# Performance work log

Hardware: AMD Instinct MI355X
Metric: run time of the kernel (lower is better)

The kernel has to match this reference:

```python
import jax, jax.numpy as jnp
import numpy as np

N_NODES = 100000
N_EDGES = 1600000
N_FEAT = 128
HIDDEN = 64
N_CLASSES = 16


def setup_inputs() -> dict:
    key = jax.random.key(0)
    ks = jax.random.split(key, 8)
    x = jax.random.normal(ks[0], (N_NODES, N_FEAT), dtype=jnp.float32)
    edge_index = jax.random.randint(ks[1], (2, N_EDGES), 0, N_NODES, dtype=jnp.int64)
    def glorot(k, shape):
        lim = float(np.sqrt(6.0 / (shape[0] + shape[1])))
        return jax.random.uniform(k, shape, jnp.float32, -lim, lim)
    return {
        "x": x,
        "edge_index": edge_index,
        "W0": glorot(ks[2], (N_FEAT, HIDDEN)), "b0": jnp.zeros((HIDDEN,), jnp.float32),
        "W1": glorot(ks[3], (HIDDEN, HIDDEN)), "b1": jnp.zeros((HIDDEN,), jnp.float32),
        "W2": glorot(ks[4], (HIDDEN, 2)),      "b2": jnp.zeros((2,), jnp.float32),
        "Wc": glorot(ks[5], (2, N_CLASSES)),   "bc": jnp.zeros((N_CLASSES,), jnp.float32),
    }


def _gcn_conv(x, W, b, src, dst, norm, n_nodes):
    # GCNConv: D^{-1/2} (A + I) D^{-1/2} X W + b, edges already include self-loops
    h = x @ W                                  # transform first (small dim)
    msg = h[src] * norm[:, None]               # gather + per-edge scale
    agg = jax.ops.segment_sum(msg, dst, num_segments=n_nodes)  # scatter-add
    return agg + b


def reference(x, edge_index, W0, b0, W1, b1, W2, b2, Wc, bc):
    n = x.shape[0]
    loops = jnp.arange(n, dtype=edge_index.dtype)
    src = jnp.concatenate([edge_index[0], loops])
    dst = jnp.concatenate([edge_index[1], loops])
    # degree on destination (col), including self-loops
    deg = jax.ops.segment_sum(jnp.ones_like(dst, dtype=x.dtype), dst, num_segments=n)
    dis = jnp.where(deg > 0, jax.lax.rsqrt(deg), 0.0)
    norm = dis[src] * dis[dst]

    h = _gcn_conv(x, W0, b0, src, dst, norm, n)              # layer 0, no activation
    h = jnp.tanh(_gcn_conv(h, W1, b1, src, dst, norm, n))    # layer 1
    h = jnp.tanh(_gcn_conv(h, W2, b2, src, dst, norm, n))    # layer 2 -> [N, 2]
    embeddings = h
    out = embeddings @ Wc + bc                               # [N, num_classes]
    return (out, embeddings)
```

## Files before the change

kernel.cpp:

```cpp
#include <hip/hip_runtime.h>


#define NF 128
#define NH 64
#define NPB 256
#define MAXNB 512
#define CAP 6144
#define A1G 1024

__global__ void k_init0(const int* __restrict__ ei, int* __restrict__ fmt,
                        int* __restrict__ ccnt, int nb16) {
    int i = blockIdx.x * 256 + threadIdx.x;
    if (i < nb16) ccnt[i] = 0;
    if (i == 0) {
        int f = 1;
        #pragma unroll
        for (int k = 1; k < 32; k += 2) if (ei[k] != 0) f = 0;
        *fmt = f;
    }
}

__global__ void __launch_bounds__(256) k_coarse(
        const int* __restrict__ ei, const int* __restrict__ fmt,
        int* __restrict__ ccnt, int* __restrict__ blockbase, int E, int NB) {
    __shared__ int h[MAXNB];
    int sh = *fmt;
    for (int i = threadIdx.x; i < NB; i += 256) h[i] = 0;
    __syncthreads();
    for (long long e = (long long)blockIdx.x * 256 + threadIdx.x; e < E;
         e += (long long)A1G * 256) {
        int d = ei[(long long)(E + e) << sh];
        atomicAdd(&h[d >> 8], 1);
    }
    __syncthreads();
    for (int b = threadIdx.x; b < NB; b += 256) {
        int c = h[b];
        int base = (c > 0) ? atomicAdd(&ccnt[b * 16], c) : 0;
        blockbase[(long long)blockIdx.x * NB + b] = base;
    }
}

__global__ void __launch_bounds__(512) k_cscan(
        const int* __restrict__ ccnt, int* __restrict__ cstart, int NB) {
    __shared__ int s[512];
    int t = threadIdx.x;
    int c = (t < NB) ? ccnt[t * 16] : 0;
    s[t] = c;
    __syncthreads();
    for (int off = 1; off < 512; off <<= 1) {
        int v = s[t];
        int u = (t >= off) ? s[t - off] : 0;
        __syncthreads();
        s[t] = v + u;
        __syncthreads();
    }
    if (t < NB) cstart[t] = s[t] - c;
}

__global__ void __launch_bounds__(256) k_cscatter(
        const int* __restrict__ ei, const int* __restrict__ fmt,
        const int* __restrict__ cstart, const int* __restrict__ blockbase,
        int* __restrict__ pairs, int E, int NB) {
    __shared__ int h[MAXNB];
    __shared__ int bb[MAXNB];
    int sh = *fmt;
    for (int i = threadIdx.x; i < NB; i += 256) {
        h[i] = 0;
        bb[i] = cstart[i] + blockbase[(long long)blockIdx.x * NB + i];
    }
    __syncthreads();
    for (long long e = (long long)blockIdx.x * 256 + threadIdx.x; e < E;
         e += (long long)A1G * 256) {
        int s = ei[(long long)e << sh];
        int d = ei[(long long)(E + e) << sh];
        int b = d >> 8;
        int r = atomicAdd(&h[b], 1);
        pairs[bb[b] + r] = s | ((d & 255) << 17);
    }
}

__global__ void __launch_bounds__(256) k_bucket(
        const int* __restrict__ pairs, const int* __restrict__ ccnt,
        const int* __restrict__ cstart, int* __restrict__ esrc,
        int* __restrict__ cnt, int* __restrict__ start, float* __restrict__ dis,
        int N) {
    __shared__ int words[CAP];
    __shared__ unsigned char rk[CAP];
    __shared__ int h[NPB];
    __shared__ int hs[NPB];
    int b = blockIdx.x;
    int cs = cstart[b];
    int ec = ccnt[b * 16];
    if (ec > CAP) ec = CAP;
    int t = threadIdx.x;
    for (int i = t; i < ec; i += 256) words[i] = pairs[cs + i];
    h[t] = 0;
    __syncthreads();
    for (int i = t; i < ec; i += 256) {
        int ld = words[i] >> 17;
        rk[i] = (unsigned char)atomicAdd(&h[ld], 1);
    }
    __syncthreads();
    int c = h[t];
    hs[t] = c;
    __syncthreads();
    for (int off = 1; off < 256; off <<= 1) {
        int v = hs[t];
        int u = (t >= off) ? hs[t - off] : 0;
        __syncthreads();
        hs[t] = v + u;
        __syncthreads();
    }
    int node = b * NPB + t;
    if (node < N) {
        cnt[node] = c;
        start[node] = cs + hs[t] - c;
        dis[node] = rsqrtf(1.0f + (float)c);
    }
    for (int i = t; i < ec; i += 256) {
        int w = words[i];
        int ld = w >> 17;
        esrc[cs + (hs[ld] - h[ld]) + rk[i]] = w & 0x1FFFF;
    }
}

#define KP3 68
__global__ void __launch_bounds__(256) k_gemm128(
        const float* __restrict__ X, const float* __restrict__ W,
        const float* __restrict__ dis, short* __restrict__ T16,
        float* __restrict__ rs, int n) {
    __shared__ float xs[64 * KP3];
    __shared__ float Ws[64 * NH];
    __shared__ int rmax[64];
    if (threadIdx.x < 64) rmax[threadIdx.x] = 0;
    long long rowbase = (long long)blockIdx.x * 64;
    int c0 = (threadIdx.x & 15) * 4;
    int r0 = (threadIdx.x >> 4) * 4;
    float4 a0{0,0,0,0}, a1{0,0,0,0}, a2{0,0,0,0}, a3{0,0,0,0};
    #pragma unroll
    for (int ph = 0; ph < 2; ++ph) {
        if (ph) __syncthreads();
        const float4* Wp4 = (const float4*)(W + (long long)ph * 64 * NH);
        for (int i = threadIdx.x; i < 64 * NH / 4; i += 256)
            ((float4*)Ws)[i] = Wp4[i];
        const float* Xp = X + rowbase * NF + ph * 64;
        for (int i = threadIdx.x; i < 1024; i += 256) {
            int r = i >> 4, kk = (i & 15) << 2;
            float4 v = (rowbase + r < n)
                           ? *(const float4*)(Xp + r * NF + kk)
                           : make_float4(0.f, 0.f, 0.f, 0.f);
            *(float4*)&xs[r * KP3 + kk] = v;
        }
        __syncthreads();
        const float* x0 = &xs[(r0 + 0) * KP3];
        const float* x1 = &xs[(r0 + 1) * KP3];
        const float* x2 = &xs[(r0 + 2) * KP3];
        const float* x3 = &xs[(r0 + 3) * KP3];
        const float* Wp0 = &Ws[c0];
        #pragma unroll 4
        for (int k4 = 0; k4 < 16; ++k4) {
            float4 xv0 = *(const float4*)(x0 + k4 * 4);
            float4 xv1 = *(const float4*)(x1 + k4 * 4);
            float4 xv2 = *(const float4*)(x2 + k4 * 4);
            float4 xv3 = *(const float4*)(x3 + k4 * 4);
            float4 wa = *(const float4*)(Wp0 + (k4 * 4 + 0) * NH);
            float4 wb = *(const float4*)(Wp0 + (k4 * 4 + 1) * NH);
            float4 wc = *(const float4*)(Wp0 + (k4 * 4 + 2) * NH);
            float4 wd = *(const float4*)(Wp0 + (k4 * 4 + 3) * NH);
            a0.x += xv0.x * wa.x; a0.y += xv0.x * wa.y; a0.z += xv0.x * wa.z; a0.w += xv0.x * wa.w;
            a1.x += xv1.x * wa.x; a1.y += xv1.x * wa.y; a1.z += xv1.x * wa.z; a1.w += xv1.x * wa.w;
            a2.x += xv2.x * wa.x; a2.y += xv2.x * wa.y; a2.z += xv2.x * wa.z; a2.w += xv2.x * wa.w;
            a3.x += xv3.x * wa.x; a3.y += xv3.x * wa.y; a3.z += xv3.x * wa.z; a3.w += xv3.x * wa.w;
            a0.x += xv0.y * wb.x; a0.y += xv0.y * wb.y; a0.z += xv0.y * wb.z; a0.w += xv0.y * wb.w;
            a1.x += xv1.y * wb.x; a1.y += xv1.y * wb.y; a1.z += xv1.y * wb.z; a1.w += xv1.y * wb.w;
            a2.x += xv2.y * wb.x; a2.y += xv2.y * wb.y; a2.z += xv2.y * wb.z; a2.w += xv2.y * wb.w;
            a3.x += xv3.y * wb.x; a3.y += xv3.y * wb.y; a3.z += xv3.y * wb.z; a3.w += xv3.y * wb.w;
            a0.x += xv0.z * wc.x; a0.y += xv0.z * wc.y; a0.z += xv0.z * wc.z; a0.w += xv0.z * wc.w;
            a1.x += xv1.z * wc.x; a1.y += xv1.z * wc.y; a1.z += xv1.z * wc.z; a1.w += xv1.z * wc.w;
            a2.x += xv2.z * wc.x; a2.y += xv2.z * wc.y; a2.z += xv2.z * wc.z; a2.w += xv2.z * wc.w;
            a3.x += xv3.z * wc.x; a3.y += xv3.z * wc.y; a3.z += xv3.z * wc.z; a3.w += xv3.z * wc.w;
            a0.x += xv0.w * wd.x; a0.y += xv0.w * wd.y; a0.z += xv0.w * wd.z; a0.w += xv0.w * wd.w;
            a1.x += xv1.w * wd.x; a1.y += xv1.w * wd.y; a1.z += xv1.w * wd.z; a1.w += xv1.w * wd.w;
            a2.x += xv2.w * wd.x; a2.y += xv2.w * wd.y; a2.z += xv2.w * wd.z; a2.w += xv2.w * wd.w;
            a3.x += xv3.w * wd.x; a3.y += xv3.w * wd.y; a3.z += xv3.w * wd.z; a3.w += xv3.w * wd.w;
        }
    }
    int row = (int)rowbase + r0;
    float d0 = (row + 0 < n) ? dis[row + 0] : 0.0f;
    float d1 = (row + 1 < n) ? dis[row + 1] : 0.0f;
    float d2 = (row + 2 < n) ? dis[row + 2] : 0.0f;
    float d3 = (row + 3 < n) ? dis[row + 3] : 0.0f;
    a0.x *= d0; a0.y *= d0; a0.z *= d0; a0.w *= d0;
    a1.x *= d1; a1.y *= d1; a1.z *= d1; a1.w *= d1;
    a2.x *= d2; a2.y *= d2; a2.z *= d2; a2.w *= d2;
    a3.x *= d3; a3.y *= d3; a3.z *= d3; a3.w *= d3;
    float m0 = fmaxf(fmaxf(fabsf(a0.x), fabsf(a0.y)), fmaxf(fabsf(a0.z), fabsf(a0.w)));
    float m1 = fmaxf(fmaxf(fabsf(a1.x), fabsf(a1.y)), fmaxf(fabsf(a1.z), fabsf(a1.w)));
    float m2 = fmaxf(fmaxf(fabsf(a2.x), fabsf(a2.y)), fmaxf(fabsf(a2.z), fabsf(a2.w)));
    float m3 = fmaxf(fmaxf(fabsf(a3.x), fabsf(a3.y)), fmaxf(fabsf(a3.z), fabsf(a3.w)));
    atomicMax(&rmax[r0 + 0], __float_as_int(m0));
    atomicMax(&rmax[r0 + 1], __float_as_int(m1));
    atomicMax(&rmax[r0 + 2], __float_as_int(m2));
    atomicMax(&rmax[r0 + 3], __float_as_int(m3));
    __syncthreads();
    float M0 = __int_as_float(rmax[r0 + 0]);
    float M1 = __int_as_float(rmax[r0 + 1]);
    float M2 = __int_as_float(rmax[r0 + 2]);
    float M3 = __int_as_float(rmax[r0 + 3]);
    float i0 = 32767.0f / fmaxf(M0, 1e-20f);
    float i1 = 32767.0f / fmaxf(M1, 1e-20f);
    float i2 = 32767.0f / fmaxf(M2, 1e-20f);
    float i3 = 32767.0f / fmaxf(M3, 1e-20f);
    const float ks = 1.0f / 32767.0f;
    if (row + 0 < n) {
        short4 q = { (short)__float2int_rn(a0.x * i0), (short)__float2int_rn(a0.y * i0),
                     (short)__float2int_rn(a0.z * i0), (short)__float2int_rn(a0.w * i0) };
        *(short4*)&T16[(long long)(row + 0) * NH + c0] = q;
        if (c0 == 0) rs[row + 0] = M0 * ks;
    }
    if (row + 1 < n) {
        short4 q = { (short)__float2int_rn(a1.x * i1), (short)__float2int_rn(a1.y * i1),
                     (short)__float2int_rn(a1.z * i1), (short)__float2int_rn(a1.w * i1) };
        *(short4*)&T16[(long long)(row + 1) * NH + c0] = q;
        if (c0 == 0) rs[row + 1] = M1 * ks;
    }
    if (row + 2 < n) {
        short4 q = { (short)__float2int_rn(a2.x * i2), (short)__float2int_rn(a2.y * i2),
                     (short)__float2int_rn(a2.z * i2), (short)__float2int_rn(a2.w * i2) };
        *(short4*)&T16[(long long)(row + 2) * NH + c0] = q;
        if (c0 == 0) rs[row + 2] = M2 * ks;
    }
    if (row + 3 < n) {
        short4 q = { (short)__float2int_rn(a3.x * i3), (short)__float2int_rn(a3.y * i3),
                     (short)__float2int_rn(a3.z * i3), (short)__float2int_rn(a3.w * i3) };
        *(short4*)&T16[(long long)(row + 3) * NH + c0] = q;
        if (c0 == 0) rs[row + 3] = M3 * ks;
    }
}

#define EDGE_A(J) {                                                           \
    int s_ = __builtin_amdgcn_readlane(sA, (J));                              \
    float f_ = __int_as_float(__builtin_amdgcn_readlane(fAb, (J)));           \
    accA = fmaf(f_, (float)(T + s_ * NH)[lane], accA); }
#define EDGE_B(J) {                                                           \
    int s_ = __builtin_amdgcn_readlane(sB, (J));                              \
    float f_ = __int_as_float(__builtin_amdgcn_readlane(fBb, (J)));           \
    accB = fmaf(f_, (float)(T + s_ * NH)[lane], accB); }

#define SEG_GATHER2                                                           \
    int lane = threadIdx.x & 63;                                              \
    int na = blockIdx.x * 8 + (threadIdx.x >> 6) * 2;                         \
    int nb_ = na + 1;                                                         \
    if (na >= n) return;                                                      \
    bool hasB = (nb_ < n);                                                    \
    float dia = dis[na];                                                      \
    float dib = hasB ? dis[nb_] : 0.0f;                                       \
    int ga = cnt[na], sta = start[na];                                        \
    int gb = hasB ? cnt[nb_] : 0;                                             \
    int stb = hasB ? start[nb_] : 0;                                          \
    float accA = rs[na] * (float)T[na * NH + lane];                           \
    float accB = hasB ? rs[nb_] * (float)T[nb_ * NH + lane] : 0.0f;           \
    int gmax = ga > gb ? ga : gb;                                             \
    for (int base = 0; base < gmax; base += 64) {                             \
        int ma = ga - base; ma = ma < 0 ? 0 : (ma > 64 ? 64 : ma);            \
        int mb = gb - base; mb = mb < 0 ? 0 : (mb > 64 ? 64 : mb);            \
        int sA = 0, sB = 0; float fA = 0.0f, fB = 0.0f;                       \
        if (lane < ma) { sA = esrc[sta + base + lane]; fA = rs[sA]; }         \
        if (lane < mb) { sB = esrc[stb + base + lane]; fB = rs[sB]; }         \
        int fAb = __float_as_int(fA), fBb = __float_as_int(fB);               \
        int mmin = ma < mb ? ma : mb;                                         \
        int j = 0;                                                            \
        for (; j + 3 < mmin; j += 4) {                                        \
            EDGE_A(j + 0) EDGE_B(j + 0)                                       \
            EDGE_A(j + 1) EDGE_B(j + 1)                                       \
            EDGE_A(j + 2) EDGE_B(j + 2)                                       \
            EDGE_A(j + 3) EDGE_B(j + 3)                                       \
        }                                                                     \
        int jA = j, jB = j;                                                   \
        for (; jA + 3 < ma; jA += 4) {                                        \
            EDGE_A(jA + 0) EDGE_A(jA + 1) EDGE_A(jA + 2) EDGE_A(jA + 3)       \
        }                                                                     \
        for (; jA < ma; ++jA) EDGE_A(jA)                                      \
        for (; jB + 3 < mb; jB += 4) {                                        \
            EDGE_B(jB + 0) EDGE_B(jB + 1) EDGE_B(jB + 2) EDGE_B(jB + 3)       \
        }                                                                     \
        for (; jB < mb; ++jB) EDGE_B(jB)                                      \
    }

__global__ void __launch_bounds__(256) k_seg0t(
        const short* __restrict__ T, const float* __restrict__ rs,
        const int* __restrict__ esrc, const int* __restrict__ start,
        const int* __restrict__ cnt, const float* __restrict__ dis,
        const float* __restrict__ b0, const float* __restrict__ W1,
        short* __restrict__ To, float* __restrict__ rso, int n) {
    __shared__ float W1s[NH * NH];
    for (int i = threadIdx.x; i < NH * NH / 4; i += 256)
        ((float4*)W1s)[i] = ((const float4*)W1)[i];
    __syncthreads();
    SEG_GATHER2
    float bv = b0[lane];
    float hA = dia * accA + bv;
    float hB = dib * accB + bv;
    float oA = 0.0f, oB = 0.0f;
    #pragma unroll
    for (int c = 0; c < 64; ++c) {
        float wv = W1s[c * NH + lane];
        float ha = __int_as_float(__builtin_amdgcn_readlane(__float_as_int(hA), c));
        float hb = __int_as_float(__builtin_amdgcn_readlane(__float_as_int(hB), c));
        oA = fmaf(ha, wv, oA);
        oB = fmaf(hb, wv, oB);
    }
    oA *= dia;
    oB *= dib;
    float mA = fabsf(oA), mB = fabsf(oB);
    #pragma unroll
    for (int msk = 32; msk; msk >>= 1) {
        mA = fmaxf(mA, __shfl_xor(mA, msk, 64));
        mB = fmaxf(mB, __shfl_xor(mB, msk, 64));
    }
    float iA = 32767.0f / fmaxf(mA, 1e-20f);
    float iB = 32767.0f / fmaxf(mB, 1e-20f);
    const float ks = 1.0f / 32767.0f;
    To[(long long)na * NH + lane] = (short)__float2int_rn(oA * iA);
    if (lane == 0) rso[na] = mA * ks;
    if (hasB) {
        To[(long long)nb_ * NH + lane] = (short)__float2int_rn(oB * iB);
        if (lane == 0) rso[nb_] = mB * ks;
    }
}

__global__ void __launch_bounds__(256) k_seg1f(
        const short* __restrict__ T, const float* __restrict__ rs,
        const int* __restrict__ esrc, const int* __restrict__ start,
        const int* __restrict__ cnt, const float* __restrict__ dis,
        const float* __restrict__ b1, const float* __restrict__ W2,
        float2* __restrict__ t2, int n) {
    SEG_GATHER2
    float bv = b1[lane];
    float2 w = ((const float2*)W2)[lane];
    float tA = tanhf(dia * accA + bv);
    float p0 = tA * w.x, p1 = tA * w.y;
    float tB = hasB ? tanhf(dib * accB + bv) : 0.0f;
    float q0 = tB * w.x, q1 = tB * w.y;
    #pragma unroll
    for (int msk = 32; msk; msk >>= 1) {
        p0 += __shfl_xor(p0, msk, 64);
        p1 += __shfl_xor(p1, msk, 64);
        q0 += __shfl_xor(q0, msk, 64);
        q1 += __shfl_xor(q1, msk, 64);
    }
    if (lane == 0) {
        t2[na] = make_float2(dia * p0, dia * p1);
        if (hasB) t2[nb_] = make_float2(dib * q0, dib * q1);
    }
}

__global__ void __launch_bounds__(256) k_seg2f(
        const float2* __restrict__ T2, const int* __restrict__ esrc,
        const int* __restrict__ start, const int* __restrict__ cnt,
        const float* __restrict__ dis, const float* __restrict__ b2,
        const float* __restrict__ Wc, const float* __restrict__ bc,
        float* __restrict__ out, float* __restrict__ emb, int n) {
    __shared__ float Wcs[32];
    __shared__ float bcs[16];
    if (threadIdx.x < 32) Wcs[threadIdx.x] = Wc[threadIdx.x];
    if (threadIdx.x < 16) bcs[threadIdx.x] = bc[threadIdx.x];
    __syncthreads();
    int i = blockIdx.x * 256 + threadIdx.x;
    if (i >= n) return;
    float di = dis[i];
    int g = cnt[i], st = start[i];
    float2 self = T2[i];
    float a0 = self.x, a1 = self.y;
    int j = 0;
    for (; j + 7 < g; j += 8) {
        int e0 = esrc[st+j],   e1 = esrc[st+j+1], e2 = esrc[st+j+2], e3 = esrc[st+j+3];
        int e4 = esrc[st+j+4], e5 = esrc[st+j+5], e6 = esrc[st+j+6], e7 = esrc[st+j+7];
        float2 v0 = T2[e0], v1 = T2[e1], v2 = T2[e2], v3 = T2[e3];
        float2 v4 = T2[e4], v5 = T2[e5], v6 = T2[e6], v7 = T2[e7];
        a0 += v0.x + v1.x + v2.x + v3.x + v4.x + v5.x + v6.x + v7.x;
        a1 += v0.y + v1.y + v2.y + v3.y + v4.y + v5.y + v6.y + v7.y;
    }
    for (; j < g; ++j) {
        float2 v = T2[esrc[st + j]];
        a0 += v.x; a1 += v.y;
    }
    float e0 = tanhf(a0 * di + b2[0]);
    float e1 = tanhf(a1 * di + b2[1]);
    *(float2*)&emb[(long long)i * 2] = make_float2(e0, e1);
    float* op = &out[(long long)i * 16];
    #pragma unroll
    for (int c4 = 0; c4 < 4; ++c4) {
        float4 o;
        o.x = e0 * Wcs[c4*4+0] + e1 * Wcs[16 + c4*4+0] + bcs[c4*4+0];
        o.y = e0 * Wcs[c4*4+1] + e1 * Wcs[16 + c4*4+1] + bcs[c4*4+1];
        o.z = e0 * Wcs[c4*4+2] + e1 * Wcs[16 + c4*4+2] + bcs[c4*4+2];
        o.w = e0 * Wcs[c4*4+3] + e1 * Wcs[16 + c4*4+3] + bcs[c4*4+3];
        *(float4*)&op[c4 * 4] = o;
    }
}

extern "C" void kernel_launch(void* const* d_in, const int* in_sizes, int n_in,
                              void* d_out, int out_size, void* d_ws, size_t ws_size,
                              hipStream_t stream) {
    const float* x  = (const float*)d_in[0];
    const int*   ei = (const int*)  d_in[1];
    const float* W0 = (const float*)d_in[2];
    const float* b0 = (const float*)d_in[3];
    const float* W1 = (const float*)d_in[4];
    const float* b1 = (const float*)d_in[5];
    const float* W2 = (const float*)d_in[6];
    const float* b2 = (const float*)d_in[7];
    const float* Wc = (const float*)d_in[8];
    const float* bc = (const float*)d_in[9];

    int N = in_sizes[0] / NF;
    int E = in_sizes[1] / 2;
    int NB = (N + NPB - 1) / NPB;

    float* out = (float*)d_out;
    float* emb = out + (long long)N * 16;

    short*  T16a = (short*)d_ws;
    char*   r2   = (char*)d_ws + (long long)N * NH * 2;
    short*  T16b = (short*)r2;
    float2* t2   = (float2*)(r2 + (long long)N * NH * 2);
    float*  rs_b = (float*)(r2 + (long long)N * NH * 2 + (long long)N * 8);
    float*  dis  = (float*)((char*)d_ws + (long long)N * NH * 2 + (long long)N * NH * 4);
    float*  rs_a = dis + N;
    int*    cnt   = (int*)(rs_a + N);
    int*    start = cnt + N;
    int*    esrc  = start + N;
    int*    fmt   = esrc + E;

    int* pairs     = (int*)d_ws;
    int* blockbase = pairs + E;
    int* ccnt      = blockbase + (long long)A1G * NB;
    int* cstart    = ccnt + NB * 16;

    int nb_n  = (N + 255) / 256;
    int nb_g  = (N + 63) / 64;
    int nb_s2 = (N + 7) / 8;
    int nb_i0 = (NB * 16 + 255) / 256;

    k_init0   <<<nb_i0, 256, 0, stream>>>(ei, fmt, ccnt, NB * 16);
    k_coarse  <<<A1G, 256, 0, stream>>>(ei, fmt, ccnt, blockbase, E, NB);
    k_cscan   <<<1, 512, 0, stream>>>(ccnt, cstart, NB);
    k_cscatter<<<A1G, 256, 0, stream>>>(ei, fmt, cstart, blockbase, pairs, E, NB);
    k_bucket  <<<NB, 256, 0, stream>>>(pairs, ccnt, cstart, esrc, cnt, start, dis, N);

    k_gemm128 <<<nb_g, 256, 0, stream>>>(x, W0, dis, T16a, rs_a, N);

    k_seg0t   <<<nb_s2, 256, 0, stream>>>(T16a, rs_a, esrc, start, cnt, dis, b0,
                                          W1, T16b, rs_b, N);

    k_seg1f   <<<nb_s2, 256, 0, stream>>>(T16b, rs_b, esrc, start, cnt, dis, b1,
                                          W2, t2, N);

    k_seg2f   <<<nb_n, 256, 0, stream>>>(t2, esrc, start, cnt, dis, b2, Wc, bc,
                                         out, emb, N);
}
```

Before: 333.3 us.

## Prefetch second GEMM phase, persistent seg0 grid, 16-lane parallel seg2 gather

The first GEMM now issues global loads for both K-halves up front, holding the second half in registers while the first is computed, and sets a 4-blocks-per-CU launch bound. The layer-1 aggregation kernel becomes grid-stride over a capped grid of 2048 blocks so the shared W1 load is amortised across many nodes. The final 2-wide aggregation spreads each node's edges across 16 lanes and combines them with shuffles, replacing one serial thread per node. These target memory-latency exposure and per-block setup, at the cost of more registers in the GEMM and less parallel slack in seg0.

```diff
diff --git a/kernel.cpp b/kernel.cpp
--- a/kernel.cpp
+++ b/kernel.cpp
@@ -124,8 +124,47 @@
     }
 }
 
+#define GEMM_K4_BODY                                                          \
+            float4 xv0 = *(const float4*)(x0 + k4 * 4);                       \
+            float4 xv1 = *(const float4*)(x1 + k4 * 4);                       \
+            float4 xv2 = *(const float4*)(x2 + k4 * 4);                       \
+            float4 xv3 = *(const float4*)(x3 + k4 * 4);                       \
+            float4 wa = *(const float4*)(Wp0 + (k4 * 4 + 0) * NH);            \
+            float4 wb = *(const float4*)(Wp0 + (k4 * 4 + 1) * NH);            \
+            float4 wc = *(const float4*)(Wp0 + (k4 * 4 + 2) * NH);            \
+            float4 wd = *(const float4*)(Wp0 + (k4 * 4 + 3) * NH);            \
+            a0.x += xv0.x * wa.x; a0.y += xv0.x * wa.y; a0.z += xv0.x * wa.z; a0.w += xv0.x * wa.w; \
+            a1.x += xv1.x * wa.x; a1.y += xv1.x * wa.y; a1.z += xv1.x * wa.z; a1.w += xv1.x * wa.w; \
+            a2.x += xv2.x * wa.x; a2.y += xv2.x * wa.y; a2.z += xv2.x * wa.z; a2.w += xv2.x * wa.w; \
+            a3.x += xv3.x * wa.x; a3.y += xv3.x * wa.y; a3.z += xv3.x * wa.z; a3.w += xv3.x * wa.w; \
+            a0.x += xv0.y * wb.x; a0.y += xv0.y * wb.y; a0.z += xv0.y * wb.z; a0.w += xv0.y * wb.w; \
+            a1.x += xv1.y * wb.x; a1.y += xv1.y * wb.y; a1.z += xv1.y * wb.z; a1.w += xv1.y * wb.w; \
+            a2.x += xv2.y * wb.x; a2.y += xv2.y * wb.y; a2.z += xv2.y * wb.z; a2.w += xv2.y * wb.w; \
+            a3.x += xv3.y * wb.x; a3.y += xv3.y * wb.y; a3.z += xv3.y * wb.z; a3.w += xv3.y * wb.w; \
+            a0.x += xv0.z * wc.x; a0.y += xv0.z * wc.y; a0.z += xv0.z * wc.z; a0.w += xv0.z * wc.w; \
+            a1.x += xv1.z * wc.x; a1.y += xv1.z * wc.y; a1.z += xv1.z * wc.z; a1.w += xv1.z * wc.w; \
+            a2.x += xv2.z * wc.x; a2.y += xv2.z * wc.y; a2.z += xv2.z * wc.z; a2.w += xv2.z * wc.w; \
+            a3.x += xv3.z * wc.x; a3.y += xv3.z * wc.y; a3.z += xv3.z * wc.z; a3.w += xv3.z * wc.w; \
+            a0.x += xv0.w * wd.x; a0.y += xv0.w * wd.y; a0.z += xv0.w * wd.z; a0.w += xv0.w * wd.w; \
+            a1.x += xv1.w * wd.x; a1.y += xv1.w * wd.y; a1.z += xv1.w * wd.z; a1.w += xv1.w * wd.w; \
+            a2.x += xv2.w * wd.x; a2.y += xv2.w * wd.y; a2.z += xv2.w * wd.z; a2.w += xv2.w * wd.w; \
+            a3.x += xv3.w * wd.x; a3.y += xv3.w * wd.y; a3.z += xv3.w * wd.z; a3.w += xv3.w * wd.w;
+
+#define GEMM_PHASE_COMPUTE                                                    \
+    {                                                                         \
+        const float* x0 = &xs[(r0 + 0) * KP3];                                \
+        const float* x1 = &xs[(r0 + 1) * KP3];                                \
+        const float* x2 = &xs[(r0 + 2) * KP3];                                \
+        const float* x3 = &xs[(r0 + 3) * KP3];                                \
+        const float* Wp0 = &Ws[c0];                                           \
+        _Pragma("unroll 4")                                                   \
+        for (int k4 = 0; k4 < 16; ++k4) {                                     \
+            GEMM_K4_BODY                                                      \
+        }                                                                     \
+    }
+
 #define KP3 68
-__global__ void __launch_bounds__(256) k_gemm128(
+__global__ void __launch_bounds__(256, 4) k_gemm128(
         const float* __restrict__ X, const float* __restrict__ W,
         const float* __restrict__ dis, short* __restrict__ T16,
         float* __restrict__ rs, int n) {
@@ -134,57 +173,43 @@
     __shared__ int rmax[64];
     if (threadIdx.x < 64) rmax[threadIdx.x] = 0;
     long long rowbase = (long long)blockIdx.x * 64;
-    int c0 = (threadIdx.x & 15) * 4;
-    int r0 = (threadIdx.x >> 4) * 4;
+    int tid = threadIdx.x;
+    int c0 = (tid & 15) * 4;
+    int r0 = (tid >> 4) * 4;
+    const float4* W4 = (const float4*)W;
+    #pragma unroll
+    for (int u = 0; u < 4; ++u) {
+        int i = tid + u * 256;
+        int r = i >> 4, kk = (i & 15) << 2;
+        float4 xv = (rowbase + r < n)
+                        ? *(const float4*)(X + (rowbase + r) * NF + kk)
+                        : make_float4(0.f, 0.f, 0.f, 0.f);
+        *(float4*)&xs[r * KP3 + kk] = xv;
+        ((float4*)Ws)[i] = W4[i];
+    }
+    float4 x1r[4], w1r[4];
+    #pragma unroll
+    for (int u = 0; u < 4; ++u) {
+        int i = tid + u * 256;
+        int r = i >> 4, kk = (i & 15) << 2;
+        x1r[u] = (rowbase + r < n)
+                     ? *(const float4*)(X + (rowbase + r) * NF + 64 + kk)
+                     : make_float4(0.f, 0.f, 0.f, 0.f);
+        w1r[u] = W4[1024 + i];
+    }
     float4 a0{0,0,0,0}, a1{0,0,0,0}, a2{0,0,0,0}, a3{0,0,0,0};
+    __syncthreads();
+    GEMM_PHASE_COMPUTE
+    __syncthreads();
     #pragma unroll
-    for (int ph = 0; ph < 2; ++ph) {
-        if (ph) __syncthreads();
-        const float4* Wp4 = (const float4*)(W + (long long)ph * 64 * NH);
-        for (int i = threadIdx.x; i < 64 * NH / 4; i += 256)
-            ((float4*)Ws)[i] = Wp4[i];
-        const float* Xp = X + rowbase * NF + ph * 64;
-        for (int i = threadIdx.x; i < 1024; i += 256) {
-            int r = i >> 4, kk = (i & 15) << 2;
-            float4 v = (rowbase + r < n)
-                           ? *(const float4*)(Xp + r * NF + kk)
-                           : make_float4(0.f, 0.f, 0.f, 0.f);
-            *(float4*)&xs[r * KP3 + kk] = v;
-        }
-        __syncthreads();
-        const float* x0 = &xs[(r0 + 0) * KP3];
-        const float* x1 = &xs[(r0 + 1) * KP3];
-        const float* x2 = &xs[(r0 + 2) * KP3];
-        const float* x3 = &xs[(r0 + 3) * KP3];
-        const float* Wp0 = &Ws[c0];
-        #pragma unroll 4
-        for (int k4 = 0; k4 < 16; ++k4) {
-            float4 xv0 = *(const float4*)(x0 + k4 * 4);
-            float4 xv1 = *(const float4*)(x1 + k4 * 4);
-            float4 xv2 = *(const float4*)(x2 + k4 * 4);
-            float4 xv3 = *(const float4*)(x3 + k4 * 4);
-            float4 wa = *(const float4*)(Wp0 + (k4 * 4 + 0) * NH);
-            float4 wb = *(const float4*)(Wp0 + (k4 * 4 + 1) * NH);
-            float4 wc = *(const float4*)(Wp0 + (k4 * 4 + 2) * NH);
-            float4 wd = *(const float4*)(Wp0 + (k4 * 4 + 3) * NH);
-            a0.x += xv0.x * wa.x; a0.y += xv0.x * wa.y; a0.z += xv0.x * wa.z; a0.w += xv0.x * wa.w;
-            a1.x += xv1.x * wa.x; a1.y += xv1.x * wa.y; a1.z += xv1.x * wa.z; a1.w += xv1.x * wa.w;
-            a2.x += xv2.x * wa.x; a2.y += xv2.x * wa.y; a2.z += xv2.x * wa.z; a2.w += xv2.x * wa.w;
-            a3.x += xv3.x * wa.x; a3.y += xv3.x * wa.y; a3.z += xv3.x * wa.z; a3.w += xv3.x * wa.w;
-            a0.x += xv0.y * wb.x; a0.y += xv0.y * wb.y; a0.z += xv0.y * wb.z; a0.w += xv0.y * wb.w;
-            a1.x += xv1.y * wb.x; a1.y += xv1.y * wb.y; a1.z += xv1.y * wb.z; a1.w += xv1.y * wb.w;
-            a2.x += xv2.y * wb.x; a2.y += xv2.y * wb.y; a2.z += xv2.y * wb.z; a2.w += xv2.y * wb.w;
-            a3.x += xv3.y * wb.x; a3.y += xv3.y * wb.y; a3.z += xv3.y * wb.z; a3.w += xv3.y * wb.w;
-            a0.x += xv0.z * wc.x; a0.y += xv0.z * wc.y; a0.z += xv0.z * wc.z; a0.w += xv0.z * wc.w;
-            a1.x += xv1.z * wc.x; a1.y += xv1.z * wc.y; a1.z += xv1.z * wc.z; a1.w += xv1.z * wc.w;
-            a2.x += xv2.z * wc.x; a2.y += xv2.z * wc.y; a2.z += xv2.z * wc.z; a2.w += xv2.z * wc.w;
-            a3.x += xv3.z * wc.x; a3.y += xv3.z * wc.y; a3.z += xv3.z * wc.z; a3.w += xv3.z * wc.w;
-            a0.x += xv0.w * wd.x; a0.y += xv0.w * wd.y; a0.z += xv0.w * wd.z; a0.w += xv0.w * wd.w;
-            a1.x += xv1.w * wd.x; a1.y += xv1.w * wd.y; a1.z += xv1.w * wd.z; a1.w += xv1.w * wd.w;
-            a2.x += xv2.w * wd.x; a2.y += xv2.w * wd.y; a2.z += xv2.w * wd.z; a2.w += xv2.w * wd.w;
-            a3.x += xv3.w * wd.x; a3.y += xv3.w * wd.y; a3.z += xv3.w * wd.z; a3.w += xv3.w * wd.w;
-        }
-    }
+    for (int u = 0; u < 4; ++u) {
+        int i = tid + u * 256;
+        int r = i >> 4, kk = (i & 15) << 2;
+        *(float4*)&xs[r * KP3 + kk] = x1r[u];
+        ((float4*)Ws)[i] = w1r[u];
+    }
+    __syncthreads();
+    GEMM_PHASE_COMPUTE
     int row = (int)rowbase + r0;
     float d0 = (row + 0 < n) ? dis[row + 0] : 0.0f;
     float d1 = (row + 1 < n) ? dis[row + 1] : 0.0f;
@@ -247,19 +272,7 @@
     float f_ = __int_as_float(__builtin_amdgcn_readlane(fBb, (J)));           \
     accB = fmaf(f_, (float)(T + s_ * NH)[lane], accB); }
 
-#define SEG_GATHER2                                                           \
-    int lane = threadIdx.x & 63;                                              \
-    int na = blockIdx.x * 8 + (threadIdx.x >> 6) * 2;                         \
-    int nb_ = na + 1;                                                         \
-    if (na >= n) return;                                                      \
-    bool hasB = (nb_ < n);                                                    \
-    float dia = dis[na];                                                      \
-    float dib = hasB ? dis[nb_] : 0.0f;                                       \
-    int ga = cnt[na], sta = start[na];                                        \
-    int gb = hasB ? cnt[nb_] : 0;                                             \
-    int stb = hasB ? start[nb_] : 0;                                          \
-    float accA = rs[na] * (float)T[na * NH + lane];                           \
-    float accB = hasB ? rs[nb_] * (float)T[nb_ * NH + lane] : 0.0f;           \
+#define GATHER_CORE                                                           \
     int gmax = ga > gb ? ga : gb;                                             \
     for (int base = 0; base < gmax; base += 64) {                             \
         int ma = ga - base; ma = ma < 0 ? 0 : (ma > 64 ? 64 : ma);            \
@@ -287,6 +300,21 @@
         for (; jB < mb; ++jB) EDGE_B(jB)                                      \
     }
 
+#define SEG_GATHER2                                                           \
+    int lane = threadIdx.x & 63;                                              \
+    int na = blockIdx.x * 8 + (threadIdx.x >> 6) * 2;                         \
+    int nb_ = na + 1;                                                         \
+    if (na >= n) return;                                                      \
+    bool hasB = (nb_ < n);                                                    \
+    float dia = dis[na];                                                      \
+    float dib = hasB ? dis[nb_] : 0.0f;                                       \
+    int ga = cnt[na], sta = start[na];                                        \
+    int gb = hasB ? cnt[nb_] : 0;                                             \
+    int stb = hasB ? start[nb_] : 0;                                          \
+    float accA = rs[na] * (float)T[na * NH + lane];                           \
+    float accB = hasB ? rs[nb_] * (float)T[nb_ * NH + lane] : 0.0f;           \
+    GATHER_CORE
+
 __global__ void __launch_bounds__(256) k_seg0t(
         const short* __restrict__ T, const float* __restrict__ rs,
         const int* __restrict__ esrc, const int* __restrict__ start,
@@ -297,35 +325,48 @@
     for (int i = threadIdx.x; i < NH * NH / 4; i += 256)
         ((float4*)W1s)[i] = ((const float4*)W1)[i];
     __syncthreads();
-    SEG_GATHER2
+    int lane = threadIdx.x & 63;
+    int wid = threadIdx.x >> 6;
     float bv = b0[lane];
-    float hA = dia * accA + bv;
-    float hB = dib * accB + bv;
-    float oA = 0.0f, oB = 0.0f;
-    #pragma unroll
-    for (int c = 0; c < 64; ++c) {
-        float wv = W1s[c * NH + lane];
-        float ha = __int_as_float(__builtin_amdgcn_readlane(__float_as_int(hA), c));
-        float hb = __int_as_float(__builtin_amdgcn_readlane(__float_as_int(hB), c));
-        oA = fmaf(ha, wv, oA);
-        oB = fmaf(hb, wv, oB);
-    }
-    oA *= dia;
-    oB *= dib;
-    float mA = fabsf(oA), mB = fabsf(oB);
-    #pragma unroll
-    for (int msk = 32; msk; msk >>= 1) {
-        mA = fmaxf(mA, __shfl_xor(mA, msk, 64));
-        mB = fmaxf(mB, __shfl_xor(mB, msk, 64));
-    }
-    float iA = 32767.0f / fmaxf(mA, 1e-20f);
-    float iB = 32767.0f / fmaxf(mB, 1e-20f);
     const float ks = 1.0f / 32767.0f;
-    To[(long long)na * NH + lane] = (short)__float2int_rn(oA * iA);
-    if (lane == 0) rso[na] = mA * ks;
-    if (hasB) {
-        To[(long long)nb_ * NH + lane] = (short)__float2int_rn(oB * iB);
-        if (lane == 0) rso[nb_] = mB * ks;
+    for (int na = blockIdx.x * 8 + wid * 2; na < n; na += gridDim.x * 8) {
+        int nb_ = na + 1;
+        bool hasB = (nb_ < n);
+        float dia = dis[na];
+        float dib = hasB ? dis[nb_] : 0.0f;
+        int ga = cnt[na], sta = start[na];
+        int gb = hasB ? cnt[nb_] : 0;
+        int stb = hasB ? start[nb_] : 0;
+        float accA = rs[na] * (float)T[(long long)na * NH + lane];
+        float accB = hasB ? rs[nb_] * (float)T[(long long)nb_ * NH + lane] : 0.0f;
+        GATHER_CORE
+        float hA = dia * accA + bv;
+        float hB = dib * accB + bv;
+        float oA = 0.0f, oB = 0.0f;
+        #pragma unroll
+        for (int c = 0; c < 64; ++c) {
+            float wv = W1s[c * NH + lane];
+            float ha = __int_as_float(__builtin_amdgcn_readlane(__float_as_int(hA), c));
+            float hb = __int_as_float(__builtin_amdgcn_readlane(__float_as_int(hB), c));
+            oA = fmaf(ha, wv, oA);
+            oB = fmaf(hb, wv, oB);
+        }
+        oA *= dia;
+        oB *= dib;
+        float mA = fabsf(oA), mB = fabsf(oB);
+        #pragma unroll
+        for (int msk = 32; msk; msk >>= 1) {
+            mA = fmaxf(mA, __shfl_xor(mA, msk, 64));
+            mB = fmaxf(mB, __shfl_xor(mB, msk, 64));
+        }
+        float iA = 32767.0f / fmaxf(mA, 1e-20f);
+        float iB = 32767.0f / fmaxf(mB, 1e-20f);
+        To[(long long)na * NH + lane] = (short)__float2int_rn(oA * iA);
+        if (lane == 0) rso[na] = mA * ks;
+        if (hasB) {
+            To[(long long)nb_ * NH + lane] = (short)__float2int_rn(oB * iB);
+            if (lane == 0) rso[nb_] = mB * ks;
+        }
     }
 }
 
@@ -361,42 +402,38 @@
         const float* __restrict__ dis, const float* __restrict__ b2,
         const float* __restrict__ Wc, const float* __restrict__ bc,
         float* __restrict__ out, float* __restrict__ emb, int n) {
-    __shared__ float Wcs[32];
-    __shared__ float bcs[16];
-    if (threadIdx.x < 32) Wcs[threadIdx.x] = Wc[threadIdx.x];
-    if (threadIdx.x < 16) bcs[threadIdx.x] = bc[threadIdx.x];
-    __syncthreads();
-    int i = blockIdx.x * 256 + threadIdx.x;
+    int lane = threadIdx.x & 63;
+    int sub = lane >> 4;
+    int sl = lane & 15;
+    int i = blockIdx.x * 16 + (threadIdx.x >> 6) * 4 + sub;
     if (i >= n) return;
     float di = dis[i];
     int g = cnt[i], st = start[i];
-    float2 self = T2[i];
-    float a0 = self.x, a1 = self.y;
-    int j = 0;
-    for (; j + 7 < g; j += 8) {
-        int e0 = esrc[st+j],   e1 = esrc[st+j+1], e2 = esrc[st+j+2], e3 = esrc[st+j+3];
-        int e4 = esrc[st+j+4], e5 = esrc[st+j+5], e6 = esrc[st+j+6], e7 = esrc[st+j+7];
-        float2 v0 = T2[e0], v1 = T2[e1], v2 = T2[e2], v3 = T2[e3];
-        float2 v4 = T2[e4], v5 = T2[e5], v6 = T2[e6], v7 = T2[e7];
-        a0 += v0.x + v1.x + v2.x + v3.x + v4.x + v5.x + v6.x + v7.x;
-        a1 += v0.y + v1.y + v2.y + v3.y + v4.y + v5.y + v6.y + v7.y;
-    }
-    for (; j < g; ++j) {
+    float a0 = 0.0f, a1 = 0.0f;
+    for (int j = sl; j < g; j += 16) {
         float2 v = T2[esrc[st + j]];
         a0 += v.x; a1 += v.y;
     }
+    if (sl == 0) {
+        float2 s = T2[i];
+        a0 += s.x; a1 += s.y;
+    }
+    #pragma unroll
+    for (int msk = 8; msk; msk >>= 1) {
+        a0 += __shfl_xor(a0, msk, 64);
+        a1 += __shfl_xor(a1, msk, 64);
+    }
     float e0 = tanhf(a0 * di + b2[0]);
     float e1 = tanhf(a1 * di + b2[1]);
-    *(float2*)&emb[(long long)i * 2] = make_float2(e0, e1);
-    float* op = &out[(long long)i * 16];
-    #pragma unroll
-    for (int c4 = 0; c4 < 4; ++c4) {
+    if (sl == 0) *(float2*)&emb[(long long)i * 2] = make_float2(e0, e1);
+    if (sl < 4) {
+        int c = sl * 4;
         float4 o;
-        o.x = e0 * Wcs[c4*4+0] + e1 * Wcs[16 + c4*4+0] + bcs[c4*4+0];
-        o.y = e0 * Wcs[c4*4+1] + e1 * Wcs[16 + c4*4+1] + bcs[c4*4+1];
-        o.z = e0 * Wcs[c4*4+2] + e1 * Wcs[16 + c4*4+2] + bcs[c4*4+2];
-        o.w = e0 * Wcs[c4*4+3] + e1 * Wcs[16 + c4*4+3] + bcs[c4*4+3];
-        *(float4*)&op[c4 * 4] = o;
+        o.x = e0 * Wc[c + 0] + e1 * Wc[16 + c + 0] + bc[c + 0];
+        o.y = e0 * Wc[c + 1] + e1 * Wc[16 + c + 1] + bc[c + 1];
+        o.z = e0 * Wc[c + 2] + e1 * Wc[16 + c + 2] + bc[c + 2];
+        o.w = e0 * Wc[c + 3] + e1 * Wc[16 + c + 3] + bc[c + 3];
+        *(float4*)&out[(long long)i * 16 + c] = o;
     }
 }
 
@@ -438,10 +475,12 @@
     int* ccnt      = blockbase + (long long)A1G * NB;
     int* cstart    = ccnt + NB * 16;
 
-    int nb_n  = (N + 255) / 256;
     int nb_g  = (N + 63) / 64;
     int nb_s2 = (N + 7) / 8;
+    int nb_2f = (N + 15) / 16;
     int nb_i0 = (NB * 16 + 255) / 256;
+    int g_seg0 = 2048;
+    if (g_seg0 > nb_s2) g_seg0 = nb_s2;
 
     k_init0   <<<nb_i0, 256, 0, stream>>>(ei, fmt, ccnt, NB * 16);
     k_coarse  <<<A1G, 256, 0, stream>>>(ei, fmt, ccnt, blockbase, E, NB);
@@ -451,12 +490,12 @@
 
     k_gemm128 <<<nb_g, 256, 0, stream>>>(x, W0, dis, T16a, rs_a, N);
 
-    k_seg0t   <<<nb_s2, 256, 0, stream>>>(T16a, rs_a, esrc, start, cnt, dis, b0,
-                                          W1, T16b, rs_b, N);
+    k_seg0t   <<<g_seg0, 256, 0, stream>>>(T16a, rs_a, esrc, start, cnt, dis, b0,
+                                           W1, T16b, rs_b, N);
 
     k_seg1f   <<<nb_s2, 256, 0, stream>>>(T16b, rs_b, esrc, start, cnt, dis, b1,
                                           W2, t2, N);
 
-    k_seg2f   <<<nb_n, 256, 0, stream>>>(t2, esrc, start, cnt, dis, b2, Wc, bc,
-                                         out, emb, N);
-}
+    k_seg2f   <<<nb_2f, 256, 0, stream>>>(t2, esrc, start, cnt, dis, b2, Wc, bc,
+                                          out, emb, N);
+}
```

Result: slower. 360.2 us (+8.1%).
